# Kernel optimization log

Hardware: AMD Instinct MI355X
Metric: run time of the kernel (lower is better)

Reference implementation:

```python
import jax, jax.numpy as jnp
import numpy as np

N_NODES = 50000
N_EDGES = 800000
N_REL = 8
HID = 256
N_BASES = 30
N_LAYERS = 2


def setup_inputs() -> dict:
    key = jax.random.key(0)
    ks = jax.random.split(key, 6)
    edge_index = jax.random.randint(ks[0], (2, N_EDGES), 0, N_NODES)
    edge_type = jax.random.randint(ks[1], (N_EDGES,), 0, N_REL)
    # learned parameters (xavier-uniform-like scales)
    s_w = (6.0 / (HID + HID)) ** 0.5
    emb = jax.random.normal(ks[2], (N_NODES, HID), dtype=jnp.float32) * 0.05
    bases = jax.random.uniform(ks[3], (N_LAYERS, N_BASES, HID, HID), dtype=jnp.float32, minval=-s_w, maxval=s_w)
    coeffs = jax.random.uniform(ks[4], (N_LAYERS, N_REL, N_BASES), dtype=jnp.float32, minval=-0.4, maxval=0.4)
    self_loops = jax.random.uniform(ks[5], (N_LAYERS, HID, HID), dtype=jnp.float32, minval=-s_w, maxval=s_w)
    return {
        "edge_index": edge_index,
        "edge_type": edge_type,
        "num_nodes": N_NODES,
        "emb": emb,
        "bases": bases,
        "coeffs": coeffs,
        "self_loops": self_loops,
    }


def reference(edge_index, edge_type, num_nodes, emb, bases, coeffs, self_loops):
    src, dst = edge_index[0], edge_index[1]
    # in-degree normalization (same every layer since graph is fixed)
    deg = jax.ops.segment_sum(jnp.ones_like(dst, dtype=emb.dtype), dst, num_segments=num_nodes)
    deg_inv = 1.0 / jnp.maximum(deg, 1.0)  # [N]

    x = emb  # embedding(arange(N)) == embedding table
    n_layers = bases.shape[0]
    for l in range(n_layers):
        # basis decomposition: W[r] = sum_b coeff[r,b] * bases[b]
        W = jnp.einsum('rb,bio->rio', coeffs[l], bases[l])        # [R, H, H]
        # transform every node by every relation (dense GEMMs), then gather per edge
        h = jnp.einsum('ni,rio->rno', x, W)                        # [R, N, H]
        msg = h[edge_type, src] * deg_inv[dst][:, None]            # [E, H]
        agg = jax.ops.segment_sum(msg, dst, num_segments=num_nodes)  # [N, H]
        x_new = agg + x @ self_loops[l]
        if l < n_layers - 1:
            x_new = jax.nn.relu(x_new)  # dropout is identity in eval mode
        x = x_new
    return x
```

## Files before the change

kernel.cpp:

```cpp
#include <hip/hip_runtime.h>
#include <hip/hip_bf16.h>

#define N_NODES 50000
#define NP 50048
#define N_EDGES 800000
#define N_REL 8
#define HID 256
#define N_BASES 30
#define SCAN_NBLK ((N_NODES + 1023) / 1024)

typedef float f4v __attribute__((ext_vector_type(4)));
typedef short sh8 __attribute__((ext_vector_type(8)));

static __device__ __forceinline__ short f2bf(float f) {
  return __builtin_bit_cast(short, __float2bfloat16(f));
}
static __device__ __forceinline__ float bf2f(unsigned short u) {
  return __builtin_bit_cast(float, ((unsigned)u) << 16);
}


__global__ void k_count(const int* __restrict__ eidx, unsigned* __restrict__ counts) {
  int e = blockIdx.x * 256 + threadIdx.x;
  if (e < N_EDGES) atomicAdd(&counts[eidx[N_EDGES + e]], 1u);
}

__global__ void k_deginv(const unsigned* __restrict__ counts, float* __restrict__ deginv) {
  int d = blockIdx.x * 256 + threadIdx.x;
  if (d < N_NODES) {
    unsigned deg = counts[d];
    deginv[d] = 1.0f / (float)(deg ? deg : 1u);
  }
}

__global__ void k_scanA(const unsigned* __restrict__ counts, unsigned* __restrict__ partials) {
  __shared__ unsigned sm[256];
  int t = threadIdx.x, b = blockIdx.x;
  int g0 = b * 1024 + t * 4;
  unsigned s = 0;
#pragma unroll
  for (int j = 0; j < 4; j++) s += (g0 + j < N_NODES) ? counts[g0 + j] : 0u;
  sm[t] = s;
  __syncthreads();
  for (int st = 128; st > 0; st >>= 1) {
    if (t < st) sm[t] += sm[t + st];
    __syncthreads();
  }
  if (t == 0) partials[b] = sm[0];
}

__global__ void k_scanB(unsigned* __restrict__ partials) {
  __shared__ unsigned sm[512];
  int t = threadIdx.x;
  unsigned v = (t < SCAN_NBLK) ? partials[t] : 0u;
  sm[t] = v;
  __syncthreads();
  for (int s = 1; s < 512; s <<= 1) {
    unsigned add = (t >= s) ? sm[t - s] : 0u;
    __syncthreads();
    sm[t] += add;
    __syncthreads();
  }
  partials[t] = sm[t] - v;
}

__global__ void k_scanC(const unsigned* __restrict__ counts, const unsigned* __restrict__ partials,
                        unsigned* __restrict__ offsets) {
  __shared__ unsigned sm[256];
  int t = threadIdx.x, b = blockIdx.x;
  int g0 = b * 1024 + t * 4;
  unsigned c[4];
#pragma unroll
  for (int j = 0; j < 4; j++) c[j] = (g0 + j < N_NODES) ? counts[g0 + j] : 0u;
  unsigned tsum = c[0] + c[1] + c[2] + c[3];
  sm[t] = tsum;
  __syncthreads();
  for (int s = 1; s < 256; s <<= 1) {
    unsigned add = (t >= s) ? sm[t - s] : 0u;
    __syncthreads();
    sm[t] += add;
    __syncthreads();
  }
  unsigned run = partials[b] + (sm[t] - tsum);
#pragma unroll
  for (int j = 0; j < 4; j++) {
    if (g0 + j < N_NODES) offsets[g0 + j] = run;
    if (g0 + j == N_NODES - 1) offsets[N_NODES] = run + c[j];
    run += c[j];
  }
}

__global__ void k_place(const int* __restrict__ eidx, const int* __restrict__ etyp,
                        const unsigned* __restrict__ offsets, unsigned* __restrict__ cursors,
                        unsigned* __restrict__ payload) {
  int e = blockIdx.x * 256 + threadIdx.x;
  if (e < N_EDGES) {
    int src = eidx[e];
    int dst = eidx[N_EDGES + e];
    int et  = etyp[e];
    unsigned pos = offsets[dst] + atomicAdd(&cursors[dst], 1u);
    payload[pos] = ((unsigned)et << 16) | (unsigned)src;
  }
}

__global__ void k_wbuild(const float* __restrict__ bases, const float* __restrict__ coeffs,
                         const float* __restrict__ selfl, short* __restrict__ Wb) {
  int bid = blockIdx.x;
  int k = bid & 255;
  int lr = bid >> 8;
  int r = lr % 9, l = lr / 9;
  int o = threadIdx.x;
  float v;
  if (r == 8) {
    v = selfl[((size_t)l * HID + k) * HID + o];
  } else {
    const float* cf = coeffs + (l * N_REL + r) * N_BASES;
    const float* bp = bases + (((size_t)l * N_BASES) * HID + k) * HID + o;
    float a = 0.f;
#pragma unroll
    for (int b = 0; b < N_BASES; b++) a += cf[b] * bp[(size_t)b * HID * HID];
    v = a;
  }
  Wb[(((size_t)l * 9 + r) * HID + o) * HID + k] = f2bf(v);
}

__global__ void k_tobf16(const float* __restrict__ src, short* __restrict__ dstp) {
  int i = blockIdx.x * 256 + threadIdx.x;
  if (i >= NP * (HID / 8)) return;
  int row = i >> 5;
  sh8 v;
  if (row < N_NODES) {
    const float* s = src + (size_t)i * 8;
    f4v a = *(const f4v*)s, b = *(const f4v*)(s + 4);
    v[0] = f2bf(a.x); v[1] = f2bf(a.y); v[2] = f2bf(a.z); v[3] = f2bf(a.w);
    v[4] = f2bf(b.x); v[5] = f2bf(b.y); v[6] = f2bf(b.z); v[7] = f2bf(b.w);
  } else {
    v = (sh8){0, 0, 0, 0, 0, 0, 0, 0};
  }
  *(sh8*)(dstp + (size_t)i * 8) = v;
}


__global__ __launch_bounds__(256, 2) void k_gemm(
    const short* __restrict__ A, const short* __restrict__ B, short* __restrict__ H,
    const int ntiles_n, const int ncols) {
  __shared__ __attribute__((aligned(16))) short As[2][128 * 64];
  __shared__ __attribute__((aligned(16))) short Bs[2][128 * 64];
  const int tid = threadIdx.x;
  const int lane = tid & 63, wv = tid >> 6;
  const int wm = wv >> 1, wn = wv & 1;
  const int llo = lane & 15, lhi = lane >> 4;
  const int mt = blockIdx.x / ntiles_n, nt = blockIdx.x % ntiles_n;
  const int m0 = mt * 128, n0 = nt * 128;

  sh8 ra[4], rb[4];
  auto LD = [&](int ks) {
#pragma unroll
    for (int i = 0; i < 4; i++) {
      int c = i * 256 + tid, row = c >> 3, s = c & 7;
      ra[i] = *(const sh8*)(A + (size_t)(m0 + row) * HID + ks * 64 + s * 8);
      rb[i] = *(const sh8*)(B + (size_t)(n0 + row) * HID + ks * 64 + s * 8);
    }
  };
  auto ST = [&](int buf) {
#pragma unroll
    for (int i = 0; i < 4; i++) {
      int c = i * 256 + tid, row = c >> 3, s = c & 7;
      int sw = s ^ (row & 7);
      *(sh8*)&As[buf][row * 64 + sw * 8] = ra[i];
      *(sh8*)&Bs[buf][row * 64 + sw * 8] = rb[i];
    }
  };

  f4v acc[4][4];
#pragma unroll
  for (int m = 0; m < 4; m++)
#pragma unroll
    for (int n = 0; n < 4; n++) acc[m][n] = (f4v){0.f, 0.f, 0.f, 0.f};

  LD(0); ST(0);
  __syncthreads();
  int cb = 0;
  for (int ks = 0; ks < 4; ks++) {
    if (ks < 3) LD(ks + 1);
#pragma unroll
    for (int kk = 0; kk < 2; kk++) {
      sh8 af[4], bfr[4];
#pragma unroll
      for (int m = 0; m < 4; m++) {
        int row = wm * 64 + m * 16 + llo;
        int kc = kk * 4 + lhi;
        af[m] = *(const sh8*)&As[cb][row * 64 + (kc ^ (row & 7)) * 8];
      }
#pragma unroll
      for (int n = 0; n < 4; n++) {
        int col = wn * 64 + n * 16 + llo;
        int kc = kk * 4 + lhi;
        bfr[n] = *(const sh8*)&Bs[cb][col * 64 + (kc ^ (col & 7)) * 8];
      }
#pragma unroll
      for (int m = 0; m < 4; m++)
#pragma unroll
        for (int n = 0; n < 4; n++)
          acc[m][n] = __builtin_amdgcn_mfma_f32_16x16x32_bf16(af[m], bfr[n], acc[m][n], 0, 0, 0);
    }
    if (ks < 3) ST(cb ^ 1);
    __syncthreads();
    cb ^= 1;
  }
#pragma unroll
  for (int m = 0; m < 4; m++)
#pragma unroll
    for (int n = 0; n < 4; n++) {
      int colg = n0 + wn * 64 + n * 16 + llo;
#pragma unroll
      for (int j = 0; j < 4; j++) {
        int rowg = m0 + wm * 64 + m * 16 + lhi * 4 + j;
        H[(size_t)rowg * ncols + colg] = f2bf(acc[m][n][j]);
      }
    }
}


__global__ __launch_bounds__(256) void k_agg(
    const short* __restrict__ H, const unsigned* __restrict__ offsets,
    const unsigned* __restrict__ payload, const float* __restrict__ deginv,
    float* __restrict__ acc_buf, short* __restrict__ x1b,
    const int cc, const int r0, const int flags) {
  const int lane = threadIdx.x & 63;
  const int wv = threadIdx.x >> 6;
  const int nw = gridDim.x * 4;
  for (int d = blockIdx.x * 4 + wv; d < NP; d += nw) {
    if (d >= N_NODES) {
      if (x1b) *(ushort4*)(x1b + (size_t)d * HID + lane * 4) = make_ushort4(0, 0, 0, 0);
      continue;
    }
    f4v acc;
    if (flags & 1) acc = (f4v){0.f, 0.f, 0.f, 0.f};
    else           acc = *(const f4v*)(acc_buf + (size_t)d * HID + lane * 4);

    unsigned p = offsets[d], e = offsets[d + 1];
    for (; p < e; p += 4) {
#pragma unroll
      for (int u = 0; u < 4; u++) {
        unsigned pp = p + u;
        unsigned pl = payload[(pp < e) ? pp : (e - 1u)];
        int et = (int)(pl >> 16) - r0;
        bool ok = (pp < e) && ((unsigned)et < (unsigned)cc);
        size_t base = ok ? ((size_t)(pl & 0xFFFFu) * cc + et) * HID : 0;
        ushort4 hv = *(const ushort4*)(H + base + lane * 4);
        float w = ok ? 1.f : 0.f;
        acc.x += w * bf2f(hv.x);
        acc.y += w * bf2f(hv.y);
        acc.z += w * bf2f(hv.z);
        acc.w += w * bf2f(hv.w);
      }
    }
    if (flags & 2) {
      float dinv = deginv[d];
      ushort4 sv = *(const ushort4*)(H + ((size_t)d * cc + (cc - 1)) * HID + lane * 4);
      f4v o;
      o.x = acc.x * dinv + bf2f(sv.x);
      o.y = acc.y * dinv + bf2f(sv.y);
      o.z = acc.z * dinv + bf2f(sv.z);
      o.w = acc.w * dinv + bf2f(sv.w);
      if (flags & 4) {
        o.x = fmaxf(o.x, 0.f); o.y = fmaxf(o.y, 0.f);
        o.z = fmaxf(o.z, 0.f); o.w = fmaxf(o.w, 0.f);
      }
      if (x1b) {
        ushort4 s4;
        s4.x = (unsigned short)f2bf(o.x); s4.y = (unsigned short)f2bf(o.y);
        s4.z = (unsigned short)f2bf(o.z); s4.w = (unsigned short)f2bf(o.w);
        *(ushort4*)(x1b + (size_t)d * HID + lane * 4) = s4;
      } else {
        *(f4v*)(acc_buf + (size_t)d * HID + lane * 4) = o;
      }
    } else {
      *(f4v*)(acc_buf + (size_t)d * HID + lane * 4) = acc;
    }
  }
}


extern "C" void kernel_launch(void* const* d_in, const int* in_sizes, int n_in,
                              void* d_out, int out_size, void* d_ws, size_t ws_size,
                              hipStream_t stream) {
  const int*   eidx   = (const int*)d_in[0];
  const int*   etyp   = (const int*)d_in[1];
  const float* emb    = (const float*)d_in[3];
  const float* bases  = (const float*)d_in[4];
  const float* coeffs = (const float*)d_in[5];
  const float* selfl  = (const float*)d_in[6];
  float* outp = (float*)d_out;
  (void)in_sizes; (void)n_in; (void)out_size;

  char* w = (char*)d_ws;
  size_t off = 0;
  auto alloc = [&](size_t bytes) -> void* {
    void* p = w + off;
    off = (off + bytes + 255) & ~(size_t)255;
    return p;
  };
  unsigned* counts   = (unsigned*)alloc((size_t)N_NODES * 4);
  unsigned* offsets  = (unsigned*)alloc((size_t)(N_NODES + 1) * 4);
  unsigned* partials = (unsigned*)alloc(512 * 4);
  float*    deginv   = (float*)alloc((size_t)N_NODES * 4);
  unsigned* payload  = (unsigned*)alloc((size_t)N_EDGES * 4);
  short*    Wb       = (short*)alloc((size_t)2 * 9 * HID * HID * 2);
  short*    xb       = (short*)alloc((size_t)NP * HID * 2);
  short*    x1b      = xb;
  const size_t per_rel = (size_t)NP * HID * 2;
  size_t avail = (ws_size > off) ? (ws_size - off) : 0;
  int crels = (int)(avail / per_rel);
  if (crels > 9) crels = 9;
  if (crels < 1) crels = 1;
  short* h = (short*)alloc(per_rel * (size_t)crels);

  hipMemsetAsync(counts, 0, (size_t)N_NODES * 4, stream);
  k_count<<<(N_EDGES + 255) / 256, 256, 0, stream>>>(eidx, counts);
  k_deginv<<<(N_NODES + 255) / 256, 256, 0, stream>>>(counts, deginv);
  k_scanA<<<SCAN_NBLK, 256, 0, stream>>>(counts, partials);
  k_scanB<<<1, 512, 0, stream>>>(partials);
  k_scanC<<<SCAN_NBLK, 256, 0, stream>>>(counts, partials, offsets);
  hipMemsetAsync(counts, 0, (size_t)N_NODES * 4, stream);
  k_place<<<(N_EDGES + 255) / 256, 256, 0, stream>>>(eidx, etyp, offsets, counts, payload);
  k_wbuild<<<2 * 9 * HID, 256, 0, stream>>>(bases, coeffs, selfl, Wb);
  k_tobf16<<<(NP * (HID / 8) + 255) / 256, 256, 0, stream>>>(emb, xb);

  for (int l = 0; l < 2; l++) {
    const short* Acur = (l == 0) ? xb : x1b;
    int r0 = 0;
    bool first = true;
    while (r0 < 9) {
      int cc = 9 - r0 < crels ? 9 - r0 : crels;
      bool fin = (r0 + cc == 9);
      k_gemm<<<391 * 2 * cc, 256, 0, stream>>>(
          Acur, Wb + ((size_t)(l * 9 + r0)) * HID * HID, h, 2 * cc, cc * HID);
      int flags = (first ? 1 : 0) | (fin ? 2 : 0) | ((l == 0 && fin) ? 4 : 0);
      k_agg<<<1024, 256, 0, stream>>>(h, offsets, payload, deginv, outp,
                                      (l == 0 && fin) ? x1b : (short*)nullptr,
                                      cc, r0, flags);
      first = false;
      r0 += cc;
    }
  }
}
```

Before: 641.8 us.

## Use direct global-to-LDS loads in GEMM and split edges across half-waves in aggregation

The GEMM staging now uses global_load_lds to copy tiles straight into shared memory, with the XOR swizzle applied on the source address. This removes the register round trip and the separate LDS store step. The aggregation kernel now has each half-wave handle alternating edges with 16-byte row loads, which doubles the edges in flight per iteration, then combines the two halves with a cross-lane shuffle. The aggregation grid is also doubled. The cost is an extra shuffle reduction per node, and the direct-to-LDS path depends on the layout mapping of lane to LDS offset being correct.

```diff
diff --git a/kernel.cpp b/kernel.cpp
--- a/kernel.cpp
+++ b/kernel.cpp
@@ -11,12 +11,17 @@
 
 typedef float f4v __attribute__((ext_vector_type(4)));
 typedef short sh8 __attribute__((ext_vector_type(8)));
+typedef unsigned short u16x8 __attribute__((ext_vector_type(8)));
 
 static __device__ __forceinline__ short f2bf(float f) {
   return __builtin_bit_cast(short, __float2bfloat16(f));
 }
 static __device__ __forceinline__ float bf2f(unsigned short u) {
   return __builtin_bit_cast(float, ((unsigned)u) << 16);
+}
+static __device__ __forceinline__ void gload16(const void* g, void* l) {
+  __builtin_amdgcn_global_load_lds((const __attribute__((address_space(1))) void*)g,
+                                   (__attribute__((address_space(3))) void*)l, 16, 0, 0);
 }
 
 
@@ -153,24 +158,18 @@
   const int mt = blockIdx.x / ntiles_n, nt = blockIdx.x % ntiles_n;
   const int m0 = mt * 128, n0 = nt * 128;
 
-  sh8 ra[4], rb[4];
-  auto LD = [&](int ks) {
+  auto STAGE = [&](int buf, int ks) {
 #pragma unroll
     for (int i = 0; i < 4; i++) {
-      int c = i * 256 + tid, row = c >> 3, s = c & 7;
-      ra[i] = *(const sh8*)(A + (size_t)(m0 + row) * HID + ks * 64 + s * 8);
-      rb[i] = *(const sh8*)(B + (size_t)(n0 + row) * HID + ks * 64 + s * 8);
+      int c = (i * 4 + wv) * 64 + lane;
+      int row = c >> 3, s = c & 7;
+      int ss = s ^ (row & 7);
+      gload16(A + (size_t)(m0 + row) * HID + ks * 64 + ss * 8,
+              &As[buf][(i * 4 + wv) * 512]);
+      gload16(B + (size_t)(n0 + row) * HID + ks * 64 + ss * 8,
+              &Bs[buf][(i * 4 + wv) * 512]);
     }
   };
-  auto ST = [&](int buf) {
-#pragma unroll
-    for (int i = 0; i < 4; i++) {
-      int c = i * 256 + tid, row = c >> 3, s = c & 7;
-      int sw = s ^ (row & 7);
-      *(sh8*)&As[buf][row * 64 + sw * 8] = ra[i];
-      *(sh8*)&Bs[buf][row * 64 + sw * 8] = rb[i];
-    }
-  };
 
   f4v acc[4][4];
 #pragma unroll
@@ -178,11 +177,11 @@
 #pragma unroll
     for (int n = 0; n < 4; n++) acc[m][n] = (f4v){0.f, 0.f, 0.f, 0.f};
 
-  LD(0); ST(0);
+  STAGE(0, 0);
   __syncthreads();
   int cb = 0;
   for (int ks = 0; ks < 4; ks++) {
-    if (ks < 3) LD(ks + 1);
+    if (ks < 3) STAGE(cb ^ 1, ks + 1);
 #pragma unroll
     for (int kk = 0; kk < 2; kk++) {
       sh8 af[4], bfr[4];
@@ -204,7 +203,6 @@
         for (int n = 0; n < 4; n++)
           acc[m][n] = __builtin_amdgcn_mfma_f32_16x16x32_bf16(af[m], bfr[n], acc[m][n], 0, 0, 0);
     }
-    if (ks < 3) ST(cb ^ 1);
     __syncthreads();
     cb ^= 1;
   }
@@ -228,42 +226,54 @@
     float* __restrict__ acc_buf, short* __restrict__ x1b,
     const int cc, const int r0, const int flags) {
   const int lane = threadIdx.x & 63;
-  const int wv = threadIdx.x >> 6;
+  const int wv   = threadIdx.x >> 6;
+  const int half = lane >> 5;
+  const int col8 = lane & 31;
+  const int col4 = col8 * 8 + half * 4;
   const int nw = gridDim.x * 4;
   for (int d = blockIdx.x * 4 + wv; d < NP; d += nw) {
     if (d >= N_NODES) {
-      if (x1b) *(ushort4*)(x1b + (size_t)d * HID + lane * 4) = make_ushort4(0, 0, 0, 0);
+      if (x1b) { ushort4 z = make_ushort4(0, 0, 0, 0);
+                 *(ushort4*)(x1b + (size_t)d * HID + col4) = z; }
       continue;
     }
-    f4v acc;
-    if (flags & 1) acc = (f4v){0.f, 0.f, 0.f, 0.f};
-    else           acc = *(const f4v*)(acc_buf + (size_t)d * HID + lane * 4);
+    float acc[8];
+    if ((flags & 1) || half) {
+#pragma unroll
+      for (int j = 0; j < 8; j++) acc[j] = 0.f;
+    } else {
+      f4v a0 = *(const f4v*)(acc_buf + (size_t)d * HID + col8 * 8);
+      f4v a1 = *(const f4v*)(acc_buf + (size_t)d * HID + col8 * 8 + 4);
+      acc[0] = a0.x; acc[1] = a0.y; acc[2] = a0.z; acc[3] = a0.w;
+      acc[4] = a1.x; acc[5] = a1.y; acc[6] = a1.z; acc[7] = a1.w;
+    }
 
     unsigned p = offsets[d], e = offsets[d + 1];
-    for (; p < e; p += 4) {
+    for (; p < e; p += 8) {
 #pragma unroll
       for (int u = 0; u < 4; u++) {
-        unsigned pp = p + u;
-        unsigned pl = payload[(pp < e) ? pp : (e - 1u)];
+        unsigned ee = p + u * 2 + (unsigned)half;
+        unsigned pl = payload[(ee < e) ? ee : (e - 1u)];
         int et = (int)(pl >> 16) - r0;
-        bool ok = (pp < e) && ((unsigned)et < (unsigned)cc);
+        bool ok = (ee < e) && ((unsigned)et < (unsigned)cc);
         size_t base = ok ? ((size_t)(pl & 0xFFFFu) * cc + et) * HID : 0;
-        ushort4 hv = *(const ushort4*)(H + base + lane * 4);
+        u16x8 hv = *(const u16x8*)(H + base + col8 * 8);
         float w = ok ? 1.f : 0.f;
-        acc.x += w * bf2f(hv.x);
-        acc.y += w * bf2f(hv.y);
-        acc.z += w * bf2f(hv.z);
-        acc.w += w * bf2f(hv.w);
-      }
-    }
+#pragma unroll
+        for (int j = 0; j < 8; j++) acc[j] += w * bf2f(hv[j]);
+      }
+    }
+#pragma unroll
+    for (int j = 0; j < 8; j++) acc[j] += __shfl_xor(acc[j], 32);
+
     if (flags & 2) {
       float dinv = deginv[d];
-      ushort4 sv = *(const ushort4*)(H + ((size_t)d * cc + (cc - 1)) * HID + lane * 4);
+      ushort4 sv = *(const ushort4*)(H + ((size_t)d * cc + (cc - 1)) * HID + col4);
       f4v o;
-      o.x = acc.x * dinv + bf2f(sv.x);
-      o.y = acc.y * dinv + bf2f(sv.y);
-      o.z = acc.z * dinv + bf2f(sv.z);
-      o.w = acc.w * dinv + bf2f(sv.w);
+      o.x = acc[half * 4 + 0] * dinv + bf2f(sv.x);
+      o.y = acc[half * 4 + 1] * dinv + bf2f(sv.y);
+      o.z = acc[half * 4 + 2] * dinv + bf2f(sv.z);
+      o.w = acc[half * 4 + 3] * dinv + bf2f(sv.w);
       if (flags & 4) {
         o.x = fmaxf(o.x, 0.f); o.y = fmaxf(o.y, 0.f);
         o.z = fmaxf(o.z, 0.f); o.w = fmaxf(o.w, 0.f);
@@ -272,12 +282,15 @@
         ushort4 s4;
         s4.x = (unsigned short)f2bf(o.x); s4.y = (unsigned short)f2bf(o.y);
         s4.z = (unsigned short)f2bf(o.z); s4.w = (unsigned short)f2bf(o.w);
-        *(ushort4*)(x1b + (size_t)d * HID + lane * 4) = s4;
+        *(ushort4*)(x1b + (size_t)d * HID + col4) = s4;
       } else {
-        *(f4v*)(acc_buf + (size_t)d * HID + lane * 4) = o;
+        *(f4v*)(acc_buf + (size_t)d * HID + col4) = o;
       }
     } else {
-      *(f4v*)(acc_buf + (size_t)d * HID + lane * 4) = acc;
+      f4v o;
+      o.x = acc[half * 4 + 0]; o.y = acc[half * 4 + 1];
+      o.z = acc[half * 4 + 2]; o.w = acc[half * 4 + 3];
+      *(f4v*)(acc_buf + (size_t)d * HID + col4) = o;
     }
   }
 }
@@ -338,7 +351,7 @@
       k_gemm<<<391 * 2 * cc, 256, 0, stream>>>(
           Acur, Wb + ((size_t)(l * 9 + r0)) * HID * HID, h, 2 * cc, cc * HID);
       int flags = (first ? 1 : 0) | (fin ? 2 : 0) | ((l == 0 && fin) ? 4 : 0);
-      k_agg<<<1024, 256, 0, stream>>>(h, offsets, payload, deginv, outp,
+      k_agg<<<2048, 256, 0, stream>>>(h, offsets, payload, deginv, outp,
                                       (l == 0 && fin) ? x1b : (short*)nullptr,
                                       cc, r0, flags);
       first = false;
```

Measured after the change: 590.6 us. -8.0%, faster.
